# Performance work log

Measured on AMD Instinct MI355X. Metric: run time of the kernel, lower is better.

## Reference

```python
import jax, jax.numpy as jnp
import numpy as np

L, D_MODEL, D_INNER, DT_RANK, D_STATE, D_CONV, VOCAB = 4, 768, 1536, 48, 16, 4, 32000
B, S = 1, 1024


def rmsnorm(x, w, eps=1e-5):
    return x * jax.lax.rsqrt(jnp.mean(x * x, axis=-1, keepdims=True) + eps) * w


def causal_depthwise_conv(x, w, b):
    # x: [B,S,D]; w: [D,1,K] (torch Conv1d groups=D weight layout); causal left-pad K-1
    y = jax.lax.conv_general_dilated(
        x.transpose(0, 2, 1), w, window_strides=(1,), padding=[(D_CONV - 1, 0)],
        dimension_numbers=('NCH', 'OIH', 'NCH'), feature_group_count=D_INNER)
    return y.transpose(0, 2, 1) + b


def selective_scan(u, dt, A, Bm, Cm, Dv):
    # Faithful to the source: A_delta = exp(dt (x) A), clamp(min=-20) is a no-op on exp output
    A_delta = jnp.clip(jnp.exp(jnp.einsum('bld,dn->bldn', dt, A)), -20.0, None)
    B_delta_u = jnp.einsum('bld,bld,bln->bldn', dt, u, Bm)
    shifted = jnp.pad(A_delta[:, 1:], ((0, 0), (1, 0), (0, 0), (0, 0)))
    A_cum = jnp.exp(jnp.cumsum(shifted, axis=1))
    h = B_delta_u / (A_cum + 1e-12)
    y = jnp.einsum('bldn,bln->bld', jnp.cumsum(h, axis=1) * A_cum, Cm)
    return y + u * Dv


def setup_inputs() -> dict:
    key = jax.random.key(0)
    ks = jax.random.split(key, 8)
    return {
        'tokens': jax.random.randint(ks[0], (B, S), 0, VOCAB),
        'embedding': jax.random.normal(ks[1], (VOCAB, D_MODEL), jnp.float32) * 0.02,
        'norm_w': jnp.ones((L, D_MODEL), jnp.float32),
        'in_proj_w': jax.random.normal(ks[2], (L, 2 * D_INNER, D_MODEL), jnp.float32) * 0.02,
        'conv_w': jax.random.normal(ks[3], (L, D_INNER, 1, D_CONV), jnp.float32) * 0.2,
        'conv_b': jnp.zeros((L, D_INNER), jnp.float32),
        'x_proj_w': jax.random.normal(ks[4], (L, DT_RANK + 2 * D_STATE, D_INNER), jnp.float32) * 0.02,
        'dt_proj_w': jax.random.normal(ks[5], (L, D_INNER, DT_RANK), jnp.float32) * 0.001,
        'dt_proj_b': jnp.full((L, D_INNER), 5.0, jnp.float32),  # delta~5 keeps exp(cumsum(exp(dt*A))) finite
        'A_log': jnp.tile(jnp.log(jnp.arange(1, D_STATE + 1, dtype=jnp.float32)), (L, D_INNER, 1)),
        'D_skip': jnp.ones((L, D_INNER), jnp.float32),
        'out_proj_w': jax.random.normal(ks[6], (L, D_MODEL, D_INNER), jnp.float32) * 0.02,
        'final_norm_w': jnp.ones((D_MODEL,), jnp.float32),
    }


def reference(tokens, embedding, norm_w, in_proj_w, conv_w, conv_b, x_proj_w,
              dt_proj_w, dt_proj_b, A_log, D_skip, out_proj_w, final_norm_w):
    x = embedding[tokens]  # [B,S,d_model]
    for i in range(L):
        h = rmsnorm(x, norm_w[i])
        xz = h @ in_proj_w[i].T                      # [B,S,2*d_inner]
        xi, res = xz[..., :D_INNER], xz[..., D_INNER:]
        xi = jax.nn.silu(causal_depthwise_conv(xi, conv_w[i], conv_b[i]))
        proj = xi @ x_proj_w[i].T                    # [B,S,dt_rank+2*d_state]
        dt = jax.nn.softplus(proj[..., :DT_RANK] @ dt_proj_w[i].T + dt_proj_b[i])
        Bm = proj[..., DT_RANK:DT_RANK + D_STATE]
        Cm = proj[..., DT_RANK + D_STATE:]
        A = -jnp.exp(A_log[i])                       # [d_inner, d_state]
        y = selective_scan(xi, dt, A, Bm, Cm, D_skip[i])
        x = x + (y * jax.nn.silu(res)) @ out_proj_w[i].T
    return rmsnorm(x, final_norm_w) @ embedding.T    # tied LM head: [B,S,vocab]
```

## Files before the change

kernel.cpp:

```cpp
#include <hip/hip_runtime.h>
#include <hip/hip_bf16.h>
#include <cmath>

namespace {

constexpr int kL      = 4;
constexpr int kDModel = 768;
constexpr int kDInner = 1536;
constexpr int kDtRank = 48;
constexpr int kDState = 16;
constexpr int kDConv  = 4;
constexpr int kSeq    = 1024;
constexpr int kPLd    = 96;
constexpr int kPB     = 128;
constexpr int kVocab  = 32000;
constexpr int kCH     = 64;
constexpr int kNCH    = kSeq / kCH;
constexpr int kDN     = kDInner * kDState;

using short8 = __attribute__((ext_vector_type(8))) short;
using f32x4  = __attribute__((ext_vector_type(4))) float;

__device__ __forceinline__ float silu_f(float v) {
    return v / (1.f + __expf(-v));
}

__device__ __forceinline__ void split_bf16(float v, __hip_bfloat16& hi, __hip_bfloat16& lo) {
    hi = __float2bfloat16(v);
    lo = __float2bfloat16(v - __bfloat162float(hi));
}

__global__ void __launch_bounds__(256) f2b_kernel(
    const float* __restrict__ src, __hip_bfloat16* __restrict__ dst, int n) {
    int i = (blockIdx.x * 256 + threadIdx.x) * 4;
    const int stride = gridDim.x * 256 * 4;
    for (; i + 3 < n; i += stride) {
        const float4 v = *reinterpret_cast<const float4*>(src + i);
        dst[i + 0] = __float2bfloat16(v.x);
        dst[i + 1] = __float2bfloat16(v.y);
        dst[i + 2] = __float2bfloat16(v.z);
        dst[i + 3] = __float2bfloat16(v.w);
    }
}

__global__ void __launch_bounds__(256) split3_kernel(
    const float* __restrict__ src, int ldsrc, int rows, int cols,
    __hip_bfloat16* __restrict__ dst, int rowsPad) {
    const int idx = blockIdx.x * 256 + threadIdx.x;
    if (idx >= rowsPad * cols) return;
    const int r = idx / cols, c = idx % cols;
    const float v = (r < rows) ? src[(size_t)r * ldsrc + c] : 0.f;
    __hip_bfloat16 hi, lo;
    split_bf16(v, hi, lo);
    __hip_bfloat16* row = dst + (size_t)r * 3 * cols;
    row[c] = hi; row[cols + c] = hi; row[2 * cols + c] = lo;
}

__global__ void __launch_bounds__(256) embed_kernel(
    const int* __restrict__ tokens, const float* __restrict__ emb,
    float* __restrict__ x) {
    const int s = blockIdx.x;
    const int t = tokens[s];
    const float* src = emb + (size_t)t * kDModel;
    float* dst = x + (size_t)s * kDModel;
    for (int d = threadIdx.x; d < kDModel; d += blockDim.x) dst[d] = src[d];
}

template <bool SPLIT>
__global__ void __launch_bounds__(256) rmsnorm_kernel(
    const float* __restrict__ x, const float* __restrict__ w,
    __hip_bfloat16* __restrict__ out) {
    const int s = blockIdx.x;
    const float* row = x + (size_t)s * kDModel;
    float ss = 0.f;
    for (int d = threadIdx.x; d < kDModel; d += blockDim.x) {
        const float v = row[d];
        ss = fmaf(v, v, ss);
    }
    #pragma unroll
    for (int m = 32; m; m >>= 1) ss += __shfl_xor(ss, m);
    __shared__ float red[4];
    if ((threadIdx.x & 63) == 0) red[threadIdx.x >> 6] = ss;
    __syncthreads();
    const float total = red[0] + red[1] + red[2] + red[3];
    const float scale = rsqrtf(total / (float)kDModel + 1e-5f);
    __hip_bfloat16* dst = out + (size_t)s * (SPLIT ? 3 * kDModel : kDModel);
    for (int d = threadIdx.x; d < kDModel; d += blockDim.x) {
        const float v = row[d] * scale * w[d];
        if (SPLIT) {
            __hip_bfloat16 hi, lo;
            split_bf16(v, hi, lo);
            dst[d] = hi; dst[kDModel + d] = lo; dst[2 * kDModel + d] = hi;
        } else {
            dst[d] = __float2bfloat16(v);
        }
    }
}

template <int BM, int BN, int KSPLIT>
__global__ void __launch_bounds__(256) mfma_gemm(
    const __hip_bfloat16* __restrict__ A, int lda,
    const __hip_bfloat16* __restrict__ B, int ldb,
    float* __restrict__ C, int ldc,
    int N, int K, size_t partStride) {
    constexpr int BK = 32;
    static_assert(BM == 128 && BN == 128, "staging assumes 128x128");
    __shared__ unsigned short As[2][BM * BK];
    __shared__ unsigned short Bs[2][BN * BK];
    const int tid  = threadIdx.x;
    const int lane = tid & 63;

    const int nwg = gridDim.x * gridDim.y;
    int bid = blockIdx.y * gridDim.x + blockIdx.x;
    {
        const int q = nwg >> 3, r = nwg & 7;
        const int xcd = bid & 7, pos = bid >> 3;
        bid = (xcd < r ? xcd * (q + 1) : r * (q + 1) + (xcd - r) * q) + pos;
    }
    const int m0 = (bid % gridDim.x) * BM;
    const int n0 = (bid / gridDim.x) * BN;

    const int Kp = K / KSPLIT;
    const int kbeg = (KSPLIT > 1) ? blockIdx.z * Kp : 0;
    float* Cw = (KSPLIT > 1) ? C + (size_t)blockIdx.z * partStride : C;
    constexpr int WM = BM / 2, WN = BN / 2;
    constexpr int MR = WM / 16, NR = WN / 16;
    const int wave = tid >> 6;
    const int wm = (wave >> 1) * WM, wn = (wave & 1) * WN;
    const int l15 = lane & 15, l4 = lane >> 4;
    f32x4 acc[MR][NR] = {};

    auto stage = [&](int buf, int k0) {
        #pragma unroll
        for (int i = 0; i < 2; ++i) {
            const int idx = tid + i * 256;
            const int r = idx >> 2, qv = idx & 3;
            const int qs = qv ^ ((r >> 1) & 3);
            __builtin_amdgcn_global_load_lds(
                (const __attribute__((address_space(1))) void*)(A + (size_t)(m0 + r) * lda + k0 + qs * 8),
                (__attribute__((address_space(3))) void*)(&As[buf][(idx - lane) * 8]),
                16, 0, 0);
        }
        #pragma unroll
        for (int i = 0; i < 2; ++i) {
            const int idx = tid + i * 256;
            const int r = idx >> 2, qv = idx & 3;
            const int qs = qv ^ ((r >> 1) & 3);
            __builtin_amdgcn_global_load_lds(
                (const __attribute__((address_space(1))) void*)(B + (size_t)(n0 + r) * ldb + k0 + qs * 8),
                (__attribute__((address_space(3))) void*)(&Bs[buf][(idx - lane) * 8]),
                16, 0, 0);
        }
    };

    const int nt = Kp / BK;
    int cur = 0;
    stage(0, kbeg);
    for (int t = 0; t < nt; ++t) {
        if (t + 1 < nt) {
            stage(cur ^ 1, kbeg + (t + 1) * BK);
            asm volatile("s_waitcnt vmcnt(4)" ::: "memory");
        } else {
            asm volatile("s_waitcnt vmcnt(0)" ::: "memory");
        }
        __builtin_amdgcn_s_barrier();

        short8 af[MR], bfv[NR];
        #pragma unroll
        for (int mi = 0; mi < MR; ++mi) {
            const int R = wm + mi * 16 + l15;
            af[mi] = *reinterpret_cast<const short8*>(&As[cur][(R * 4 + (l4 ^ ((R >> 1) & 3))) * 8]);
        }
        #pragma unroll
        for (int ni = 0; ni < NR; ++ni) {
            const int R = wn + ni * 16 + l15;
            bfv[ni] = *reinterpret_cast<const short8*>(&Bs[cur][(R * 4 + (l4 ^ ((R >> 1) & 3))) * 8]);
        }
        #pragma unroll
        for (int mi = 0; mi < MR; ++mi)
            #pragma unroll
            for (int ni = 0; ni < NR; ++ni)
                acc[mi][ni] = __builtin_amdgcn_mfma_f32_16x16x32_bf16(
                    af[mi], bfv[ni], acc[mi][ni], 0, 0, 0);

        asm volatile("s_waitcnt lgkmcnt(0)" ::: "memory");
        __builtin_amdgcn_s_barrier();
        cur ^= 1;
    }

    #pragma unroll
    for (int mi = 0; mi < MR; ++mi) {
        const int mrow = m0 + wm + mi * 16 + l4 * 4;
        #pragma unroll
        for (int ni = 0; ni < NR; ++ni) {
            const int ncol = n0 + wn + ni * 16 + l15;
            if (ncol >= N) continue;
            #pragma unroll
            for (int r = 0; r < 4; ++r)
                Cw[(size_t)(mrow + r) * ldc + ncol] = acc[mi][ni][r];
        }
    }
}

template <int NP, bool ADD>
__global__ void __launch_bounds__(256) reduce_parts(
    const float* __restrict__ parts, size_t stride,
    float* __restrict__ dst, int count) {
    const int i = (blockIdx.x * 256 + threadIdx.x) * 4;
    if (i >= count) return;
    float4 s = *reinterpret_cast<const float4*>(parts + i);
    #pragma unroll
    for (int p = 1; p < NP; ++p) {
        const float4 v = *reinterpret_cast<const float4*>(parts + (size_t)p * stride + i);
        s.x += v.x; s.y += v.y; s.z += v.z; s.w += v.w;
    }
    float4* d = reinterpret_cast<float4*>(dst + i);
    if (ADD) {
        float4 o = *d;
        o.x += s.x; o.y += s.y; o.z += s.z; o.w += s.w;
        *d = o;
    } else {
        *d = s;
    }
}

__global__ void __launch_bounds__(256) dt_kernel(
    const float* __restrict__ proj, const float* __restrict__ dtw,
    const float* __restrict__ bias, float* __restrict__ dt) {
    __shared__ float sw[kDtRank][257];
    const int tid = threadIdx.x;
    const int n0 = blockIdx.x * 256;
    const int m0 = blockIdx.y * 8;
    for (int idx = tid; idx < 256 * kDtRank; idx += 256) {
        const int nn = idx / kDtRank, k = idx % kDtRank;
        sw[k][nn] = dtw[(size_t)(n0 + nn) * kDtRank + k];
    }
    __syncthreads();
    const int n = n0 + tid;
    const float b = bias[n];
    #pragma unroll
    for (int mi = 0; mi < 8; ++mi) {
        const float* pr = proj + (size_t)(m0 + mi) * kPLd;
        float acc = b;
        #pragma unroll
        for (int k = 0; k < kDtRank; ++k)
            acc = fmaf(pr[k], sw[k][tid], acc);
        acc = (acc > 20.f) ? acc : log1pf(__expf(acc));
        dt[(size_t)(m0 + mi) * kDInner + n] = acc;
    }
}

__global__ void __launch_bounds__(256) conv_silu_kernel(
    const float* __restrict__ p0, const float* __restrict__ p1,
    const float* __restrict__ cw, const float* __restrict__ cb,
    float* __restrict__ xi, __hip_bfloat16* __restrict__ xi2) {
    const int s = blockIdx.x;
    const int d = blockIdx.y * 256 + threadIdx.x;
    float acc = cb[d];
    #pragma unroll
    for (int k = 0; k < kDConv; ++k) {
        const int sl = s - (kDConv - 1) + k;
        if (sl >= 0) {
            const size_t off = (size_t)sl * (2 * kDInner) + d;
            acc = fmaf(p0[off] + p1[off], cw[d * kDConv + k], acc);
        }
    }
    const float v = silu_f(acc);
    xi[(size_t)s * kDInner + d] = v;
    __hip_bfloat16 hi, lo;
    split_bf16(v, hi, lo);
    __hip_bfloat16* row = xi2 + (size_t)s * 3 * kDInner;
    row[d] = hi; row[kDInner + d] = lo; row[2 * kDInner + d] = hi;
}

__global__ void __launch_bounds__(256) scan_part1(
    const float* __restrict__ dt, const float* __restrict__ u,
    const float* __restrict__ proj, const float* __restrict__ A_log,
    float* __restrict__ P, float* __restrict__ S) {
    __shared__ float sdt[kCH][16], su[kCH][16], sB[kCH][16];
    const int tid = threadIdx.x;
    const int n = tid & 15, dl = tid >> 4;
    const int d0 = blockIdx.x * 16;
    const int l0 = blockIdx.y * kCH;
    for (int idx = tid; idx < kCH * 16; idx += 256) {
        const int r = idx >> 4, c = idx & 15;
        sdt[r][c] = dt[(size_t)(l0 + r) * kDInner + d0 + c];
        su [r][c] = u [(size_t)(l0 + r) * kDInner + d0 + c];
        sB [r][c] = proj[(size_t)(l0 + r) * kPLd + kDtRank + c];
    }
    __syncthreads();
    const int d = d0 + dl;
    const float Adn = -__expf(A_log[d * kDState + n]);
    float state = 0.f, sumA = 0.f;
    #pragma unroll 8
    for (int l = 0; l < kCH; ++l) {
        const float dtv = sdt[l][dl];
        const float adelta = __expf(dtv * Adn);
        const float mult = __expf(adelta);
        state = fmaf(state, mult, dtv * su[l][dl] * sB[l][n]);
        sumA += adelta;
    }
    const int dn = d * kDState + n;
    P[(size_t)blockIdx.y * kDN + dn] = __expf(sumA);
    S[(size_t)blockIdx.y * kDN + dn] = state;
}

__global__ void __launch_bounds__(256) scan_combine(
    const float* __restrict__ P, const float* __restrict__ S,
    float* __restrict__ SI) {
    const int dn = blockIdx.x * 256 + threadIdx.x;
    float s = 0.f;
    #pragma unroll
    for (int j = 0; j < kNCH; ++j) {
        const size_t idx = (size_t)j * kDN + dn;
        SI[idx] = s;
        s = fmaf(s, P[idx], S[idx]);
    }
}

__global__ void __launch_bounds__(256) scan_part2(
    const float* __restrict__ dt, const float* __restrict__ u,
    const float* __restrict__ proj, const float* __restrict__ A_log,
    const float* __restrict__ D_skip, const float* __restrict__ SI,
    float* __restrict__ y) {
    __shared__ float sdt[kCH][16], su[kCH][16], sB[kCH][16], sC[kCH][16];
    __shared__ float sy[kCH][16];
    const int tid = threadIdx.x;
    const int n = tid & 15, dl = tid >> 4;
    const int d0 = blockIdx.x * 16;
    const int l0 = blockIdx.y * kCH;
    for (int idx = tid; idx < kCH * 16; idx += 256) {
        const int r = idx >> 4, c = idx & 15;
        sdt[r][c] = dt[(size_t)(l0 + r) * kDInner + d0 + c];
        su [r][c] = u [(size_t)(l0 + r) * kDInner + d0 + c];
        sB [r][c] = proj[(size_t)(l0 + r) * kPLd + kDtRank + c];
        sC [r][c] = proj[(size_t)(l0 + r) * kPLd + kDtRank + kDState + c];
    }
    __syncthreads();
    const int d = d0 + dl;
    const float Adn = -__expf(A_log[d * kDState + n]);
    const float Dv  = D_skip[d];
    float state = SI[(size_t)blockIdx.y * kDN + d * kDState + n];
    for (int l = 0; l < kCH; ++l) {
        const float dtv = sdt[l][dl];
        const float uv  = su[l][dl];
        const float mult = __expf(__expf(dtv * Adn));
        state = fmaf(state, mult, dtv * uv * sB[l][n]);
        float contrib = state * sC[l][n];
        contrib += __shfl_xor(contrib, 8);
        contrib += __shfl_xor(contrib, 4);
        contrib += __shfl_xor(contrib, 2);
        contrib += __shfl_xor(contrib, 1);
        if (n == 0) sy[l][dl] = fmaf(uv, Dv, contrib);
    }
    __syncthreads();
    for (int idx = tid; idx < kCH * 16; idx += 256) {
        const int r = idx >> 4, c = idx & 15;
        y[(size_t)(l0 + r) * kDInner + d0 + c] = sy[r][c];
    }
}

__global__ void __launch_bounds__(256) mul_silu_kernel(
    const float* __restrict__ y, const float* __restrict__ p0,
    const float* __restrict__ p1, __hip_bfloat16* __restrict__ g2) {
    const int s = blockIdx.x;
    const int d = blockIdx.y * 256 + threadIdx.x;
    const size_t off = (size_t)s * (2 * kDInner) + kDInner + d;
    const float res = p0[off] + p1[off];
    const float v = y[(size_t)s * kDInner + d] * silu_f(res);
    __hip_bfloat16 hi, lo;
    split_bf16(v, hi, lo);
    __hip_bfloat16* row = g2 + (size_t)s * 3 * kDInner;
    row[d] = hi; row[kDInner + d] = lo; row[2 * kDInner + d] = hi;
}

}

extern "C" void kernel_launch(void* const* d_in, const int* in_sizes, int n_in,
                              void* d_out, int out_size, void* d_ws, size_t ws_size,
                              hipStream_t stream) {
    const int*   tokens       = (const int*)d_in[0];
    const float* embedding    = (const float*)d_in[1];
    const float* norm_w       = (const float*)d_in[2];
    const float* in_proj_w    = (const float*)d_in[3];
    const float* conv_w       = (const float*)d_in[4];
    const float* conv_b       = (const float*)d_in[5];
    const float* x_proj_w     = (const float*)d_in[6];
    const float* dt_proj_w    = (const float*)d_in[7];
    const float* dt_proj_b    = (const float*)d_in[8];
    const float* A_log        = (const float*)d_in[9];
    const float* D_skip       = (const float*)d_in[10];
    const float* out_proj_w   = (const float*)d_in[11];
    const float* final_norm_w = (const float*)d_in[12];
    float* out = (float*)d_out;

    constexpr int K3m = 3 * kDModel;
    constexpr int K3i = 3 * kDInner;

    char* ws = (char*)d_ws;
    auto alloc = [&](size_t bytes) { char* p = ws; ws += (bytes + 255) & ~(size_t)255; return p; };
    float* x    = (float*)alloc((size_t)kSeq * kDModel * 4);
    float* xi   = (float*)alloc((size_t)kSeq * kDInner * 4);
    float* proj = (float*)alloc((size_t)kSeq * kPLd * 4);
    float* dt   = (float*)alloc((size_t)kSeq * kDInner * 4);
    float* y    = (float*)alloc((size_t)kSeq * kDInner * 4);
    float* scanP  = (float*)alloc((size_t)kNCH * kDN * 4);
    float* scanS  = (float*)alloc((size_t)kNCH * kDN * 4);
    float* scanSI = (float*)alloc((size_t)kNCH * kDN * 4);
    float* partsXZ = (float*)alloc((size_t)2 * kSeq * 2 * kDInner * 4);
    float* partsP  = (float*)alloc((size_t)16 * kSeq * kPLd * 4);
    float* partsO  = (float*)alloc((size_t)4 * kSeq * kDModel * 4);
    __hip_bfloat16* h_bf   = (__hip_bfloat16*)alloc((size_t)kSeq * kDModel * 2);
    __hip_bfloat16* h2     = (__hip_bfloat16*)alloc((size_t)kSeq * K3m * 2);
    __hip_bfloat16* xi2    = (__hip_bfloat16*)alloc((size_t)kSeq * K3i * 2);
    __hip_bfloat16* g2     = (__hip_bfloat16*)alloc((size_t)kSeq * K3i * 2);
    __hip_bfloat16* emb_bf = (__hip_bfloat16*)alloc((size_t)kVocab * kDModel * 2);
    __hip_bfloat16* inw2   = (__hip_bfloat16*)alloc((size_t)kL * 2 * kDInner * K3m * 2);
    __hip_bfloat16* outw2  = (__hip_bfloat16*)alloc((size_t)kL * kDModel * K3i * 2);
    __hip_bfloat16* xw2    = (__hip_bfloat16*)alloc((size_t)kL * kPB * K3i * 2);

    f2b_kernel<<<4096, 256, 0, stream>>>(embedding, emb_bf, kVocab * kDModel);
    split3_kernel<<<(kL * 2 * kDInner * kDModel + 255) / 256, 256, 0, stream>>>(
        in_proj_w, kDModel, kL * 2 * kDInner, kDModel, inw2, kL * 2 * kDInner);
    split3_kernel<<<(kL * kDModel * kDInner + 255) / 256, 256, 0, stream>>>(
        out_proj_w, kDInner, kL * kDModel, kDInner, outw2, kL * kDModel);
    for (int i = 0; i < kL; ++i)
        split3_kernel<<<(kPB * kDInner + 255) / 256, 256, 0, stream>>>(
            x_proj_w + (size_t)i * (kDtRank + 2 * kDState) * kDInner, kDInner,
            kDtRank + 2 * kDState, kDInner, xw2 + (size_t)i * kPB * K3i, kPB);

    embed_kernel<<<kSeq, 256, 0, stream>>>(tokens, embedding, x);

    for (int i = 0; i < kL; ++i) {
        rmsnorm_kernel<true><<<kSeq, 256, 0, stream>>>(x, norm_w + (size_t)i * kDModel, h2);

        mfma_gemm<128, 128, 2><<<dim3(kSeq / 128, 2 * kDInner / 128, 2), 256, 0, stream>>>(
            h2, K3m, inw2 + (size_t)i * 2 * kDInner * K3m, K3m,
            partsXZ, 2 * kDInner, 2 * kDInner, K3m, (size_t)kSeq * 2 * kDInner);

        conv_silu_kernel<<<dim3(kSeq, kDInner / 256), 256, 0, stream>>>(
            partsXZ, partsXZ + (size_t)kSeq * 2 * kDInner,
            conv_w + (size_t)i * kDInner * kDConv, conv_b + (size_t)i * kDInner,
            xi, xi2);

        mfma_gemm<128, 128, 16><<<dim3(kSeq / 128, 1, 16), 256, 0, stream>>>(
            xi2, K3i, xw2 + (size_t)i * kPB * K3i, K3i,
            partsP, kPLd, kPLd, K3i, (size_t)kSeq * kPLd);
        reduce_parts<16, false><<<(kSeq * kPLd / 4 + 255) / 256, 256, 0, stream>>>(
            partsP, (size_t)kSeq * kPLd, proj, kSeq * kPLd);

        dt_kernel<<<dim3(kDInner / 256, kSeq / 8), 256, 0, stream>>>(
            proj, dt_proj_w + (size_t)i * kDInner * kDtRank,
            dt_proj_b + (size_t)i * kDInner, dt);

        const float* A_l = A_log + (size_t)i * kDInner * kDState;
        scan_part1<<<dim3(kDInner / 16, kNCH), 256, 0, stream>>>(
            dt, xi, proj, A_l, scanP, scanS);
        scan_combine<<<kDN / 256, 256, 0, stream>>>(scanP, scanS, scanSI);
        scan_part2<<<dim3(kDInner / 16, kNCH), 256, 0, stream>>>(
            dt, xi, proj, A_l, D_skip + (size_t)i * kDInner, scanSI, y);

        mul_silu_kernel<<<dim3(kSeq, kDInner / 256), 256, 0, stream>>>(
            y, partsXZ, partsXZ + (size_t)kSeq * 2 * kDInner, g2);

        mfma_gemm<128, 128, 4><<<dim3(kSeq / 128, kDModel / 128, 4), 256, 0, stream>>>(
            g2, K3i, outw2 + (size_t)i * kDModel * K3i, K3i,
            partsO, kDModel, kDModel, K3i, (size_t)kSeq * kDModel);
        reduce_parts<4, true><<<(kSeq * kDModel / 4 + 255) / 256, 256, 0, stream>>>(
            partsO, (size_t)kSeq * kDModel, x, kSeq * kDModel);
    }

    rmsnorm_kernel<false><<<kSeq, 256, 0, stream>>>(x, final_norm_w, h_bf);
    mfma_gemm<128, 128, 1><<<dim3(kSeq / 128, kVocab / 128, 1), 256, 0, stream>>>(
        h_bf, kDModel, emb_bf, kDModel, out, kVocab, kVocab, kDModel, 0);
}
```

Measured before the change: 851.7 us.

## Use 128x256 LM-head tiles, raise split-K, fold scan combine into part2

Generalizes the MFMA GEMM to 512-thread 128x256 tiles and uses that shape for the vocab projection, aiming to improve operand reuse on the largest GEMM. The K-split of the x_proj and out_proj GEMMs goes up (16→24, 4→6) for more parallelism, with larger partial buffers and more reduction traffic. The scan_combine kernel is removed: each scan_part2 block now recomputes its chunk-prefix state serially from P/S. This saves a launch and a buffer but adds redundant prefix work in later chunks.

```diff
diff --git a/kernel.cpp b/kernel.cpp
--- a/kernel.cpp
+++ b/kernel.cpp
@@ -98,13 +98,17 @@
 }
 
 template <int BM, int BN, int KSPLIT>
-__global__ void __launch_bounds__(256) mfma_gemm(
+__global__ void __launch_bounds__((BN == 256) ? 512 : 256) mfma_gemm(
     const __hip_bfloat16* __restrict__ A, int lda,
     const __hip_bfloat16* __restrict__ B, int ldb,
     float* __restrict__ C, int ldc,
     int N, int K, size_t partStride) {
     constexpr int BK = 32;
-    static_assert(BM == 128 && BN == 128, "staging assumes 128x128");
+    constexpr int THREADS = (BN == 256) ? 512 : 256;
+    constexpr int WAVES_M = 2;
+    constexpr int WAVES_N = THREADS / 64 / WAVES_M;
+    constexpr int LPT = (BM * 4 + BN * 4) / THREADS;
+    static_assert(BM == 128, "A staging assumes BM=128");
     __shared__ unsigned short As[2][BM * BK];
     __shared__ unsigned short Bs[2][BN * BK];
     const int tid  = threadIdx.x;
@@ -123,17 +127,17 @@
     const int Kp = K / KSPLIT;
     const int kbeg = (KSPLIT > 1) ? blockIdx.z * Kp : 0;
     float* Cw = (KSPLIT > 1) ? C + (size_t)blockIdx.z * partStride : C;
-    constexpr int WM = BM / 2, WN = BN / 2;
+    constexpr int WM = BM / WAVES_M, WN = BN / WAVES_N;
     constexpr int MR = WM / 16, NR = WN / 16;
     const int wave = tid >> 6;
-    const int wm = (wave >> 1) * WM, wn = (wave & 1) * WN;
+    const int wm = (wave / WAVES_N) * WM, wn = (wave % WAVES_N) * WN;
     const int l15 = lane & 15, l4 = lane >> 4;
     f32x4 acc[MR][NR] = {};
 
     auto stage = [&](int buf, int k0) {
         #pragma unroll
-        for (int i = 0; i < 2; ++i) {
-            const int idx = tid + i * 256;
+        for (int i = 0; i < BM * 4 / THREADS; ++i) {
+            const int idx = tid + i * THREADS;
             const int r = idx >> 2, qv = idx & 3;
             const int qs = qv ^ ((r >> 1) & 3);
             __builtin_amdgcn_global_load_lds(
@@ -142,8 +146,8 @@
                 16, 0, 0);
         }
         #pragma unroll
-        for (int i = 0; i < 2; ++i) {
-            const int idx = tid + i * 256;
+        for (int i = 0; i < BN * 4 / THREADS; ++i) {
+            const int idx = tid + i * THREADS;
             const int r = idx >> 2, qv = idx & 3;
             const int qs = qv ^ ((r >> 1) & 3);
             __builtin_amdgcn_global_load_lds(
@@ -159,7 +163,8 @@
     for (int t = 0; t < nt; ++t) {
         if (t + 1 < nt) {
             stage(cur ^ 1, kbeg + (t + 1) * BK);
-            asm volatile("s_waitcnt vmcnt(4)" ::: "memory");
+            if constexpr (LPT == 4) asm volatile("s_waitcnt vmcnt(4)" ::: "memory");
+            else                    asm volatile("s_waitcnt vmcnt(3)" ::: "memory");
         } else {
             asm volatile("s_waitcnt vmcnt(0)" ::: "memory");
         }
@@ -305,24 +310,11 @@
     S[(size_t)blockIdx.y * kDN + dn] = state;
 }
 
-__global__ void __launch_bounds__(256) scan_combine(
-    const float* __restrict__ P, const float* __restrict__ S,
-    float* __restrict__ SI) {
-    const int dn = blockIdx.x * 256 + threadIdx.x;
-    float s = 0.f;
-    #pragma unroll
-    for (int j = 0; j < kNCH; ++j) {
-        const size_t idx = (size_t)j * kDN + dn;
-        SI[idx] = s;
-        s = fmaf(s, P[idx], S[idx]);
-    }
-}
-
 __global__ void __launch_bounds__(256) scan_part2(
     const float* __restrict__ dt, const float* __restrict__ u,
     const float* __restrict__ proj, const float* __restrict__ A_log,
-    const float* __restrict__ D_skip, const float* __restrict__ SI,
-    float* __restrict__ y) {
+    const float* __restrict__ D_skip, const float* __restrict__ P,
+    const float* __restrict__ S, float* __restrict__ y) {
     __shared__ float sdt[kCH][16], su[kCH][16], sB[kCH][16], sC[kCH][16];
     __shared__ float sy[kCH][16];
     const int tid = threadIdx.x;
@@ -336,11 +328,16 @@
         sB [r][c] = proj[(size_t)(l0 + r) * kPLd + kDtRank + c];
         sC [r][c] = proj[(size_t)(l0 + r) * kPLd + kDtRank + kDState + c];
     }
+    const int dn = d0 * kDState + tid;
+    float state = 0.f;
+    for (int jj = 0; jj < (int)blockIdx.y; ++jj) {
+        const size_t idx = (size_t)jj * kDN + dn;
+        state = fmaf(state, P[idx], S[idx]);
+    }
     __syncthreads();
     const int d = d0 + dl;
     const float Adn = -__expf(A_log[d * kDState + n]);
     const float Dv  = D_skip[d];
-    float state = SI[(size_t)blockIdx.y * kDN + d * kDState + n];
     for (int l = 0; l < kCH; ++l) {
         const float dtv = sdt[l][dl];
         const float uv  = su[l][dl];
@@ -406,10 +403,9 @@
     float* y    = (float*)alloc((size_t)kSeq * kDInner * 4);
     float* scanP  = (float*)alloc((size_t)kNCH * kDN * 4);
     float* scanS  = (float*)alloc((size_t)kNCH * kDN * 4);
-    float* scanSI = (float*)alloc((size_t)kNCH * kDN * 4);
     float* partsXZ = (float*)alloc((size_t)2 * kSeq * 2 * kDInner * 4);
-    float* partsP  = (float*)alloc((size_t)16 * kSeq * kPLd * 4);
-    float* partsO  = (float*)alloc((size_t)4 * kSeq * kDModel * 4);
+    float* partsP  = (float*)alloc((size_t)24 * kSeq * kPLd * 4);
+    float* partsO  = (float*)alloc((size_t)6 * kSeq * kDModel * 4);
     __hip_bfloat16* h_bf   = (__hip_bfloat16*)alloc((size_t)kSeq * kDModel * 2);
     __hip_bfloat16* h2     = (__hip_bfloat16*)alloc((size_t)kSeq * K3m * 2);
     __hip_bfloat16* xi2    = (__hip_bfloat16*)alloc((size_t)kSeq * K3i * 2);
@@ -443,10 +439,10 @@
             conv_w + (size_t)i * kDInner * kDConv, conv_b + (size_t)i * kDInner,
             xi, xi2);
 
-        mfma_gemm<128, 128, 16><<<dim3(kSeq / 128, 1, 16), 256, 0, stream>>>(
+        mfma_gemm<128, 128, 24><<<dim3(kSeq / 128, 1, 24), 256, 0, stream>>>(
             xi2, K3i, xw2 + (size_t)i * kPB * K3i, K3i,
             partsP, kPLd, kPLd, K3i, (size_t)kSeq * kPLd);
-        reduce_parts<16, false><<<(kSeq * kPLd / 4 + 255) / 256, 256, 0, stream>>>(
+        reduce_parts<24, false><<<(kSeq * kPLd / 4 + 255) / 256, 256, 0, stream>>>(
             partsP, (size_t)kSeq * kPLd, proj, kSeq * kPLd);
 
         dt_kernel<<<dim3(kDInner / 256, kSeq / 8), 256, 0, stream>>>(
@@ -456,21 +452,20 @@
         const float* A_l = A_log + (size_t)i * kDInner * kDState;
         scan_part1<<<dim3(kDInner / 16, kNCH), 256, 0, stream>>>(
             dt, xi, proj, A_l, scanP, scanS);
-        scan_combine<<<kDN / 256, 256, 0, stream>>>(scanP, scanS, scanSI);
         scan_part2<<<dim3(kDInner / 16, kNCH), 256, 0, stream>>>(
-            dt, xi, proj, A_l, D_skip + (size_t)i * kDInner, scanSI, y);
+            dt, xi, proj, A_l, D_skip + (size_t)i * kDInner, scanP, scanS, y);
 
         mul_silu_kernel<<<dim3(kSeq, kDInner / 256), 256, 0, stream>>>(
             y, partsXZ, partsXZ + (size_t)kSeq * 2 * kDInner, g2);
 
-        mfma_gemm<128, 128, 4><<<dim3(kSeq / 128, kDModel / 128, 4), 256, 0, stream>>>(
+        mfma_gemm<128, 128, 6><<<dim3(kSeq / 128, kDModel / 128, 6), 256, 0, stream>>>(
             g2, K3i, outw2 + (size_t)i * kDModel * K3i, K3i,
             partsO, kDModel, kDModel, K3i, (size_t)kSeq * kDModel);
-        reduce_parts<4, true><<<(kSeq * kDModel / 4 + 255) / 256, 256, 0, stream>>>(
+        reduce_parts<6, true><<<(kSeq * kDModel / 4 + 255) / 256, 256, 0, stream>>>(
             partsO, (size_t)kSeq * kDModel, x, kSeq * kDModel);
     }
 
     rmsnorm_kernel<false><<<kSeq, 256, 0, stream>>>(x, final_norm_w, h_bf);
-    mfma_gemm<128, 128, 1><<<dim3(kSeq / 128, kVocab / 128, 1), 256, 0, stream>>>(
+    mfma_gemm<128, 256, 1><<<dim3(kSeq / 128, kVocab / 256, 1), 512, 0, stream>>>(
         h_bf, kDModel, emb_bf, kDModel, out, kVocab, kVocab, kDModel, 0);
 }
```

New measurement: 822.5 us. 3.4% less time.
